# Kernel tuning notes

Measured on AMD Instinct MI355X. Metric: run time of the kernel, lower is better.

The kernel has to match this reference:

```python
import jax, jax.numpy as jnp
import numpy as np

N_QUBITS = 10
N_LAYERS = 2
BATCH = 4096


def _apply_1q(state, U, w):
    """Apply a single-qubit gate U ((2,2) or (batch,2,2)) on wire w.
    state: (batch, 2,2,...,2) with axis w+1 for wire w (wire 0 = leftmost)."""
    s = jnp.moveaxis(state, w + 1, -1)
    if U.ndim == 2:
        s = jnp.einsum('ij,...j->...i', U, s)
    else:  # per-sample gate (AngleEmbedding)
        s = jnp.einsum('bij,b...j->b...i', U, s)
    return jnp.moveaxis(s, -1, w + 1)


def _apply_cnot(state, c, t):
    ax_c, ax_t = c + 1, t + 1
    s0 = jnp.take(state, jnp.array([0]), axis=ax_c)
    s1 = jnp.take(state, jnp.array([1]), axis=ax_c)
    s1 = jnp.flip(s1, axis=ax_t)  # X on target where control == 1
    return jnp.concatenate([s0, s1], axis=ax_c)


def _ry(theta):
    """RY gate; theta scalar -> (2,2), theta (batch,) -> (batch,2,2)."""
    c, s = jnp.cos(theta / 2), jnp.sin(theta / 2)
    return jnp.stack([jnp.stack([c, -s], -1), jnp.stack([s, c], -1)], -2).astype(jnp.complex64)


def _rot(phi, theta, omega):
    """PennyLane Rot(phi, theta, omega) = RZ(omega) @ RY(theta) @ RZ(phi)."""
    c, s = jnp.cos(theta / 2), jnp.sin(theta / 2)
    ep = jnp.exp(-0.5j * (phi + omega))
    em = jnp.exp(0.5j * (phi - omega))
    return jnp.stack([
        jnp.stack([ep * c, -em * s], -1),
        jnp.stack([jnp.conj(em) * s, jnp.conj(ep) * c], -1),
    ], -2).astype(jnp.complex64)


def _qcircuit(x, weights):
    batch, n = x.shape
    L = weights.shape[0]
    state = jnp.zeros((batch,) + (2,) * n, dtype=jnp.complex64)
    state = state.at[(slice(None),) + (0,) * n].set(1.0)
    # AngleEmbedding, rotation='Y'
    for w in range(n):
        state = _apply_1q(state, _ry(x[:, w]), w)
    # StronglyEntanglingLayers: Rot on each wire, then CNOT ring with range r
    for l in range(L):
        for w in range(n):
            state = _apply_1q(state, _rot(weights[l, w, 0], weights[l, w, 1], weights[l, w, 2]), w)
        r = (l % (n - 1)) + 1
        for w in range(n):
            state = _apply_cnot(state, w, (w + r) % n)
    probs = state.real ** 2 + state.imag ** 2
    zs = []
    for w in range(n):
        axes = tuple(a for a in range(1, n + 1) if a != w + 1)
        m = probs.sum(axis=axes)  # (batch, 2)
        zs.append(m[:, 0] - m[:, 1])  # <Z_w>
    return jnp.stack(zs, axis=1).astype(jnp.float32)  # (batch, n)


def setup_inputs() -> dict:
    key = jax.random.key(0)
    ks = jax.random.split(key, 6)
    x = jax.random.uniform(ks[0], (BATCH, N_QUBITS), dtype=jnp.float32, maxval=2 * np.pi)
    weights = jax.random.uniform(ks[1], (N_LAYERS, N_QUBITS, 3), dtype=jnp.float32, maxval=2 * np.pi)
    w1 = jax.random.normal(ks[2], (8, N_QUBITS), dtype=jnp.float32) * 0.3
    b1 = jax.random.normal(ks[3], (8,), dtype=jnp.float32) * 0.1
    w2 = jax.random.normal(ks[4], (1, 8), dtype=jnp.float32) * 0.3
    b2 = jax.random.normal(ks[5], (1,), dtype=jnp.float32) * 0.1
    return {"x": x, "weights": weights, "w1": w1, "b1": b1, "w2": w2, "b2": b2}


def reference(x, weights, w1, b1, w2, b2):
    q = _qcircuit(x, weights)                 # (batch, n_qubits)
    h = jax.nn.relu(q @ w1.T + b1)            # (batch, 8)
    return jax.nn.sigmoid(h @ w2.T + b2)      # (batch, 1)
```

## Files before the change

### kernel.cpp

```cpp
#include <hip/hip_runtime.h>
#include <math.h>

#define NQ 10
#define BATCH 4096


struct CR { int c, t, flip; };
__host__ __device__ constexpr CR cnot_conj(int lc, int lt) {
    const int xc = lc & 1, zc = (lc >> 1) & 1;
    const int xt = lt & 1, zt = (lt >> 1) & 1;
    const int flip = xc & zt & ((xt ^ zc) ^ 1);
    const int nxt = xt ^ xc;
    const int nzc = zc ^ zt;
    return { (nzc << 1) | xc, (zt << 1) | nxt, flip };
}

template<int SM, int K, int L1, int L0, int F>
__device__ __forceinline__ float chain(const float (&B)[NQ][4], const float (&C)[NQ][4], float p) {
    if constexpr (K == 0) {
        constexpr CR r = cnot_conj(L0, L1);
        float v = p;
        if constexpr (r.t != 0) v *= B[1][r.t];
        if constexpr (r.c != 0) v *= B[0][r.c];
        if constexpr (F ^ r.flip) return -v; else return v;
    } else if constexpr ((SM >> K) & 1) {
        float s = 0.f;
        {   constexpr CR r = cnot_conj(1, L1);
            float p2 = p * C[K][1];
            if constexpr (r.t != 0) p2 *= B[K + 1][r.t];
            s += chain<SM, K - 1, r.c, L0, F ^ r.flip>(B, C, p2); }
        {   constexpr CR r = cnot_conj(2, L1);
            float p2 = p * C[K][2];
            if constexpr (r.t != 0) p2 *= B[K + 1][r.t];
            s += chain<SM, K - 1, r.c, L0, F ^ r.flip>(B, C, p2); }
        {   constexpr CR r = cnot_conj(3, L1);
            float p2 = p * C[K][3];
            if constexpr (r.t != 0) p2 *= B[K + 1][r.t];
            s += chain<SM, K - 1, r.c, L0, F ^ r.flip>(B, C, p2); }
        return s;
    } else {
        constexpr CR r = cnot_conj(0, L1);
        float p2 = p;
        if constexpr (r.t != 0) p2 *= B[K + 1][r.t];
        return chain<SM, K - 1, r.c, L0, F ^ r.flip>(B, C, p2);
    }
}

template<int SM, int S0, int S9>
__device__ __forceinline__ float top2(const float (&B)[NQ][4], const float (&C)[NQ][4]) {
    constexpr CR r = cnot_conj(S9, S0);
    float p = 1.f;
    if constexpr (S0 != 0) p *= C[0][S0];
    if constexpr (S9 != 0) p *= C[9][S9];
    return chain<SM, 8, r.c, r.t, r.flip>(B, C, p);
}
template<int SM, int S0>
__device__ __forceinline__ float sum9(const float (&B)[NQ][4], const float (&C)[NQ][4]) {
    if constexpr ((SM >> 9) & 1)
        return top2<SM, S0, 1>(B, C) + top2<SM, S0, 2>(B, C) + top2<SM, S0, 3>(B, C);
    else
        return top2<SM, S0, 0>(B, C);
}
template<int SM>
__device__ __forceinline__ float obs_eval(const float (&B)[NQ][4], const float (&C)[NQ][4]) {
    if constexpr (SM & 1)
        return sum9<SM, 1>(B, C) + sum9<SM, 2>(B, C) + sum9<SM, 3>(B, C);
    else
        return sum9<SM, 0>(B, C);
}

__global__ __launch_bounds__(256) void qnn_kernel(
    const float* __restrict__ x, const float* __restrict__ weights,
    const float* __restrict__ w1, const float* __restrict__ b1,
    const float* __restrict__ w2, const float* __restrict__ b2,
    float* __restrict__ out)
{
    __shared__ float U[60];
    __shared__ float CCs[40];
    __shared__ float zb[64 * 11];

    const int t = threadIdx.x;

    if (t < NQ) {
        float phi0 = weights[t * 3 + 0], th0 = weights[t * 3 + 1], om0 = weights[t * 3 + 2];
        float phi1 = weights[(NQ + t) * 3 + 0], th1 = weights[(NQ + t) * 3 + 1];
        float cp, sp_, co, so, ct, st;
        sincosf(phi0, &sp_, &cp);
        sincosf(th0,  &st,  &ct);
        sincosf(om0,  &so,  &co);
        U[t * 6 + 0] = co * ct * cp - so * sp_;
        U[t * 6 + 1] = so * ct * cp + co * sp_;
        U[t * 6 + 2] = -st * cp;
        U[t * 6 + 3] = co * st;
        U[t * 6 + 4] = so * st;
        U[t * 6 + 5] = ct;
        float c1p, s1p, c1t, s1t;
        sincosf(phi1, &s1p, &c1p);
        sincosf(th1,  &s1t, &c1t);
        CCs[t * 4 + 1] = -s1t * c1p;
        CCs[t * 4 + 2] =  c1t;
        CCs[t * 4 + 3] =  s1t * s1p;
    }
    __syncthreads();

    const int g    = t >> 6;
    const int lane = t & 63;
    const int sample = blockIdx.x * 64 + lane;

    float B[NQ][4];
    float C[NQ][4];
    const float2* xp = (const float2*)(x + sample * NQ);
    #pragma unroll
    for (int h = 0; h < 5; ++h) {
        float2 xv = xp[h];
        #pragma unroll
        for (int q2 = 0; q2 < 2; ++q2) {
            int w = 2 * h + q2;
            float sx, cx;
            __sincosf(q2 ? xv.y : xv.x, &sx, &cx);
            B[w][0] = 1.f;
            B[w][1] = fmaf(sx, U[w * 6 + 0], cx * U[w * 6 + 3]);
            B[w][3] = fmaf(sx, U[w * 6 + 1], cx * U[w * 6 + 4]);
            B[w][2] = fmaf(sx, U[w * 6 + 2], cx * U[w * 6 + 5]);
            C[w][0] = 1.f;
            C[w][1] = CCs[w * 4 + 1];
            C[w][2] = CCs[w * 4 + 2];
            C[w][3] = CCs[w * 4 + 3];
        }
    }

    float* zrow = zb + lane * 11;
    if (g == 0) {
        zrow[8] = obs_eval<0x155>(B, C);
        zrow[2] = obs_eval<0x005>(B, C);
    } else if (g == 1) {
        zrow[9] = obs_eval<0x2AA>(B, C);
        zrow[3] = obs_eval<0x00A>(B, C);
    } else if (g == 2) {
        zrow[0] = obs_eval<0x154>(B, C);
        zrow[6] = obs_eval<0x055>(B, C);
        zrow[4] = obs_eval<0x015>(B, C);
    } else {
        zrow[1] = obs_eval<0x2A8>(B, C);
        zrow[7] = obs_eval<0x0AA>(B, C);
        zrow[5] = obs_eval<0x02A>(B, C);
    }
    __syncthreads();

    if (g == 0) {
        float z[NQ];
        #pragma unroll
        for (int w = 0; w < NQ; ++w) z[w] = zb[lane * 11 + w];
        float acc2 = b2[0];
        #pragma unroll
        for (int j = 0; j < 8; ++j) {
            float h = b1[j];
            #pragma unroll
            for (int w = 0; w < NQ; ++w)
                h = fmaf(z[w], w1[j * NQ + w], h);
            h = fmaxf(h, 0.f);
            acc2 = fmaf(h, w2[j], acc2);
        }
        out[sample] = 1.f / (1.f + __expf(-acc2));
    }
}

extern "C" void kernel_launch(void* const* d_in, const int* in_sizes, int n_in,
                              void* d_out, int out_size, void* d_ws, size_t ws_size,
                              hipStream_t stream) {
    const float* x       = (const float*)d_in[0];
    const float* weights = (const float*)d_in[1];
    const float* w1      = (const float*)d_in[2];
    const float* b1      = (const float*)d_in[3];
    const float* w2      = (const float*)d_in[4];
    const float* b2      = (const float*)d_in[5];
    float* out = (float*)d_out;

    qnn_kernel<<<BATCH / 64, 256, 0, stream>>>(x, weights, w1, b1, w2, b2, out);
}
```

Baseline: 67.70 us.

## Split observable tree evaluation across more blocks and add separate MLP kernel

```diff
diff --git a/kernel.cpp b/kernel.cpp
--- a/kernel.cpp
+++ b/kernel.cpp
@@ -69,15 +69,12 @@
         return sum9<SM, 0>(B, C);
 }
 
-__global__ __launch_bounds__(256) void qnn_kernel(
+__global__ __launch_bounds__(256) void tree_kernel(
     const float* __restrict__ x, const float* __restrict__ weights,
-    const float* __restrict__ w1, const float* __restrict__ b1,
-    const float* __restrict__ w2, const float* __restrict__ b2,
-    float* __restrict__ out)
+    float* __restrict__ zpart)
 {
     __shared__ float U[60];
     __shared__ float CCs[40];
-    __shared__ float zb[64 * 11];
 
     const int t = threadIdx.x;
 
@@ -105,7 +102,9 @@
 
     const int g    = t >> 6;
     const int lane = t & 63;
-    const int sample = blockIdx.x * 64 + lane;
+    const int sg   = blockIdx.x >> 2;
+    const int ob   = blockIdx.x & 3;
+    const int sample = sg * 64 + lane;
 
     float B[NQ][4];
     float C[NQ][4];
@@ -129,40 +128,63 @@
         }
     }
 
-    float* zrow = zb + lane * 11;
-    if (g == 0) {
-        zrow[8] = obs_eval<0x155>(B, C);
-        zrow[2] = obs_eval<0x005>(B, C);
-    } else if (g == 1) {
-        zrow[9] = obs_eval<0x2AA>(B, C);
-        zrow[3] = obs_eval<0x00A>(B, C);
-    } else if (g == 2) {
-        zrow[0] = obs_eval<0x154>(B, C);
-        zrow[6] = obs_eval<0x055>(B, C);
-        zrow[4] = obs_eval<0x015>(B, C);
+    float v = 0.f;
+    bool has = true;
+    if (ob == 0) {
+        if      (g == 0) v = sum9<0x155, 1>(B, C);
+        else if (g == 1) v = sum9<0x155, 2>(B, C);
+        else if (g == 2) v = sum9<0x155, 3>(B, C);
+        else             v = obs_eval<0x005>(B, C);
+    } else if (ob == 1) {
+        if      (g == 0) v = top2<0x2AA, 0, 1>(B, C);
+        else if (g == 1) v = top2<0x2AA, 0, 2>(B, C);
+        else if (g == 2) v = top2<0x2AA, 0, 3>(B, C);
+        else             v = obs_eval<0x00A>(B, C);
+    } else if (ob == 2) {
+        if      (g == 0) v = obs_eval<0x154>(B, C);
+        else if (g == 1) v = obs_eval<0x2A8>(B, C);
+        else if (g == 2) v = obs_eval<0x015>(B, C);
+        else             v = obs_eval<0x02A>(B, C);
     } else {
-        zrow[1] = obs_eval<0x2A8>(B, C);
-        zrow[7] = obs_eval<0x0AA>(B, C);
-        zrow[5] = obs_eval<0x02A>(B, C);
-    }
-    __syncthreads();
-
-    if (g == 0) {
-        float z[NQ];
+        if      (g == 0) v = obs_eval<0x055>(B, C);
+        else if (g == 1) v = obs_eval<0x0AA>(B, C);
+        else             has = false;
+    }
+    if (has)
+        zpart[(ob * 4 + g) * BATCH + sample] = v;
+}
+
+__global__ __launch_bounds__(256) void mlp_kernel(
+    const float* __restrict__ zpart,
+    const float* __restrict__ w1, const float* __restrict__ b1,
+    const float* __restrict__ w2, const float* __restrict__ b2,
+    float* __restrict__ out)
+{
+    const int s = blockIdx.x * 256 + threadIdx.x;
+
+    float z[NQ];
+    z[8] = (zpart[0 * BATCH + s] + zpart[1 * BATCH + s]) + zpart[2 * BATCH + s];
+    z[2] =  zpart[3 * BATCH + s];
+    z[9] = (zpart[4 * BATCH + s] + zpart[5 * BATCH + s]) + zpart[6 * BATCH + s];
+    z[3] =  zpart[7 * BATCH + s];
+    z[0] =  zpart[8 * BATCH + s];
+    z[1] =  zpart[9 * BATCH + s];
+    z[4] =  zpart[10 * BATCH + s];
+    z[5] =  zpart[11 * BATCH + s];
+    z[6] =  zpart[12 * BATCH + s];
+    z[7] =  zpart[13 * BATCH + s];
+
+    float acc2 = b2[0];
+    #pragma unroll
+    for (int j = 0; j < 8; ++j) {
+        float h = b1[j];
         #pragma unroll
-        for (int w = 0; w < NQ; ++w) z[w] = zb[lane * 11 + w];
-        float acc2 = b2[0];
-        #pragma unroll
-        for (int j = 0; j < 8; ++j) {
-            float h = b1[j];
-            #pragma unroll
-            for (int w = 0; w < NQ; ++w)
-                h = fmaf(z[w], w1[j * NQ + w], h);
-            h = fmaxf(h, 0.f);
-            acc2 = fmaf(h, w2[j], acc2);
-        }
-        out[sample] = 1.f / (1.f + __expf(-acc2));
-    }
+        for (int w = 0; w < NQ; ++w)
+            h = fmaf(z[w], w1[j * NQ + w], h);
+        h = fmaxf(h, 0.f);
+        acc2 = fmaf(h, w2[j], acc2);
+    }
+    out[s] = 1.f / (1.f + __expf(-acc2));
 }
 
 extern "C" void kernel_launch(void* const* d_in, const int* in_sizes, int n_in,
@@ -174,7 +196,9 @@
     const float* b1      = (const float*)d_in[3];
     const float* w2      = (const float*)d_in[4];
     const float* b2      = (const float*)d_in[5];
-    float* out = (float*)d_out;
-
-    qnn_kernel<<<BATCH / 64, 256, 0, stream>>>(x, weights, w1, b1, w2, b2, out);
-}
+    float* out   = (float*)d_out;
+    float* zpart = (float*)d_ws;
+
+    tree_kernel<<<64 * 4, 256, 0, stream>>>(x, weights, zpart);
+    mlp_kernel<<<BATCH / 256, 256, 0, stream>>>(zpart, w1, b1, w2, b2, out);
+}
```

Measured after the change: 67.57 us (median of 2 runs). No clear change (-0.2%).

## Split observable evaluation across 14 wavefronts per block for load balance

Applied to the files above, without the earlier changes.

```diff
diff --git a/kernel.cpp b/kernel.cpp
--- a/kernel.cpp
+++ b/kernel.cpp
@@ -69,7 +69,7 @@
         return sum9<SM, 0>(B, C);
 }
 
-__global__ __launch_bounds__(256) void qnn_kernel(
+__global__ __launch_bounds__(1024) void qnn_kernel(
     const float* __restrict__ x, const float* __restrict__ weights,
     const float* __restrict__ w1, const float* __restrict__ b1,
     const float* __restrict__ w2, const float* __restrict__ b2,
@@ -77,7 +77,7 @@
 {
     __shared__ float U[60];
     __shared__ float CCs[40];
-    __shared__ float zb[64 * 11];
+    __shared__ float zp[14 * 64];
 
     const int t = threadIdx.x;
 
@@ -107,50 +107,63 @@
     const int lane = t & 63;
     const int sample = blockIdx.x * 64 + lane;
 
-    float B[NQ][4];
-    float C[NQ][4];
-    const float2* xp = (const float2*)(x + sample * NQ);
-    #pragma unroll
-    for (int h = 0; h < 5; ++h) {
-        float2 xv = xp[h];
+    if (g < 14) {
+        float B[NQ][4];
+        float C[NQ][4];
+        const float2* xp = (const float2*)(x + sample * NQ);
         #pragma unroll
-        for (int q2 = 0; q2 < 2; ++q2) {
-            int w = 2 * h + q2;
-            float sx, cx;
-            __sincosf(q2 ? xv.y : xv.x, &sx, &cx);
-            B[w][0] = 1.f;
-            B[w][1] = fmaf(sx, U[w * 6 + 0], cx * U[w * 6 + 3]);
-            B[w][3] = fmaf(sx, U[w * 6 + 1], cx * U[w * 6 + 4]);
-            B[w][2] = fmaf(sx, U[w * 6 + 2], cx * U[w * 6 + 5]);
-            C[w][0] = 1.f;
-            C[w][1] = CCs[w * 4 + 1];
-            C[w][2] = CCs[w * 4 + 2];
-            C[w][3] = CCs[w * 4 + 3];
+        for (int h = 0; h < 5; ++h) {
+            float2 xv = xp[h];
+            #pragma unroll
+            for (int q2 = 0; q2 < 2; ++q2) {
+                int w = 2 * h + q2;
+                float sx, cx;
+                __sincosf(q2 ? xv.y : xv.x, &sx, &cx);
+                B[w][0] = 1.f;
+                B[w][1] = fmaf(sx, U[w * 6 + 0], cx * U[w * 6 + 3]);
+                B[w][3] = fmaf(sx, U[w * 6 + 1], cx * U[w * 6 + 4]);
+                B[w][2] = fmaf(sx, U[w * 6 + 2], cx * U[w * 6 + 5]);
+                C[w][0] = 1.f;
+                C[w][1] = CCs[w * 4 + 1];
+                C[w][2] = CCs[w * 4 + 2];
+                C[w][3] = CCs[w * 4 + 3];
+            }
         }
-    }
 
-    float* zrow = zb + lane * 11;
-    if (g == 0) {
-        zrow[8] = obs_eval<0x155>(B, C);
-        zrow[2] = obs_eval<0x005>(B, C);
-    } else if (g == 1) {
-        zrow[9] = obs_eval<0x2AA>(B, C);
-        zrow[3] = obs_eval<0x00A>(B, C);
-    } else if (g == 2) {
-        zrow[0] = obs_eval<0x154>(B, C);
-        zrow[6] = obs_eval<0x055>(B, C);
-        zrow[4] = obs_eval<0x015>(B, C);
-    } else {
-        zrow[1] = obs_eval<0x2A8>(B, C);
-        zrow[7] = obs_eval<0x0AA>(B, C);
-        zrow[5] = obs_eval<0x02A>(B, C);
+        float v;
+        switch (g) {
+            case 0:  v = sum9<0x155, 1>(B, C);    break;
+            case 1:  v = sum9<0x155, 2>(B, C);    break;
+            case 2:  v = sum9<0x155, 3>(B, C);    break;
+            case 3:  v = obs_eval<0x005>(B, C);   break;
+            case 4:  v = top2<0x2AA, 0, 1>(B, C); break;
+            case 5:  v = top2<0x2AA, 0, 2>(B, C); break;
+            case 6:  v = top2<0x2AA, 0, 3>(B, C); break;
+            case 7:  v = obs_eval<0x00A>(B, C);   break;
+            case 8:  v = obs_eval<0x154>(B, C);   break;
+            case 9:  v = obs_eval<0x2A8>(B, C);   break;
+            case 10: v = obs_eval<0x015>(B, C);   break;
+            case 11: v = obs_eval<0x02A>(B, C);   break;
+            case 12: v = obs_eval<0x055>(B, C);   break;
+            default: v = obs_eval<0x0AA>(B, C);   break;
+        }
+        zp[g * 64 + lane] = v;
     }
     __syncthreads();
 
     if (g == 0) {
         float z[NQ];
-        #pragma unroll
-        for (int w = 0; w < NQ; ++w) z[w] = zb[lane * 11 + w];
+        z[8] = (zp[0 * 64 + lane] + zp[1 * 64 + lane]) + zp[2 * 64 + lane];
+        z[2] =  zp[3 * 64 + lane];
+        z[9] = (zp[4 * 64 + lane] + zp[5 * 64 + lane]) + zp[6 * 64 + lane];
+        z[3] =  zp[7 * 64 + lane];
+        z[0] =  zp[8 * 64 + lane];
+        z[1] =  zp[9 * 64 + lane];
+        z[4] =  zp[10 * 64 + lane];
+        z[5] =  zp[11 * 64 + lane];
+        z[6] =  zp[12 * 64 + lane];
+        z[7] =  zp[13 * 64 + lane];
+
         float acc2 = b2[0];
         #pragma unroll
         for (int j = 0; j < 8; ++j) {
@@ -176,5 +189,5 @@
     const float* b2      = (const float*)d_in[5];
     float* out = (float*)d_out;
 
-    qnn_kernel<<<BATCH / 64, 256, 0, stream>>>(x, weights, w1, b1, w2, b2, out);
+    qnn_kernel<<<BATCH / 64, 1024, 0, stream>>>(x, weights, w1, b1, w2, b2, out);
 }
```

Measured after the change: 68.80 us. No clear change (+1.6%).
